# Kernel optimization log

Measured on AMD Instinct MI355X. Metric: run time of the kernel, lower is better.

## Reference

```python
import jax, jax.numpy as jnp
import numpy as np

N_ROWS = 524288   # total ragged rows (sum of lengths)
N_SEG = 128       # number of segments (batch of ragged sequences)
N_FEAT = 256      # num_features
EPS = 1e-05


def setup_inputs() -> dict:
    key = jax.random.key(0)
    k_x = jax.random.fold_in(key, 1)
    x = jax.random.normal(k_x, (N_ROWS, N_FEAT), dtype=jnp.float32)
    # ragged lengths: strictly positive, sum exactly N_ROWS
    rng = np.random.default_rng(0)
    boundaries = np.sort(rng.choice(np.arange(1, N_ROWS), size=N_SEG - 1, replace=False))
    lengths_np = np.diff(np.concatenate([[0], boundaries, [N_ROWS]])).astype(np.int64)
    lengths = jnp.asarray(lengths_np)
    weight = jnp.ones((N_FEAT,), dtype=jnp.float32)
    bias = jnp.zeros((N_FEAT,), dtype=jnp.float32)
    return {"x": x, "lengths": lengths, "weight": weight, "bias": bias}


def reference(x, lengths, weight, bias):
    # instance norm over ragged segments: per-segment, per-feature mean/var
    B = lengths.shape[0]
    seg_ids = jnp.repeat(jnp.arange(B, dtype=jnp.int32), lengths,
                         total_repeat_length=x.shape[0])      # [N]
    cnt = lengths.astype(x.dtype)[:, None]                    # [B,1]
    mean = jax.ops.segment_sum(x, seg_ids, num_segments=B) / cnt          # [B,F]
    x_centered = x - mean[seg_ids]                                        # [N,F]
    var = jax.ops.segment_sum(x_centered * x_centered, seg_ids,
                              num_segments=B) / cnt                       # [B,F]
    std = jnp.sqrt(var + EPS)                                             # [B,F]
    x_norm = x_centered / std[seg_ids]                                    # [N,F]
    return x_norm * weight + bias
```

## Files before the change

### kernel.cpp

```cpp
#include <hip/hip_runtime.h>

#define NFEAT 256
#define NQ    64
#define CH    256
#define BLK   256

typedef float f32x4_native __attribute__((ext_vector_type(4)));

__device__ __forceinline__ void nt_store4(float4* p, float4 v) {
    f32x4_native n; n.x = v.x; n.y = v.y; n.z = v.z; n.w = v.w;
    __builtin_nontemporal_store(n, reinterpret_cast<f32x4_native*>(p));
}

__device__ __forceinline__ void block_scan(const int* __restrict__ lengths, int B,
                                           int* soff, int* sbs) {
    __shared__ int L[BLK], C[BLK];
    const int t = threadIdx.x;
    int len = (t < B) ? lengths[t] : 0;
    L[t] = len;
    C[t] = (len + CH - 1) / CH;
    __syncthreads();
    #pragma unroll
    for (int d = 1; d < BLK; d <<= 1) {
        int a = L[t], c = C[t], aa = 0, cc = 0;
        if (t >= d) { aa = L[t - d]; cc = C[t - d]; }
        __syncthreads();
        L[t] = a + aa; C[t] = c + cc;
        __syncthreads();
    }
    if (t == 0) { soff[0] = 0; sbs[0] = 0; }
    if (t < B)  { soff[t + 1] = L[t]; sbs[t + 1] = C[t]; }
    __syncthreads();
}

__device__ __forceinline__ int find_seg(const int* __restrict__ sbs, int B, int c) {
    __shared__ int sseg;
    const int t = threadIdx.x;
    if (t < B && sbs[t] <= c && c < sbs[t + 1]) sseg = t;
    __syncthreads();
    return sseg;
}

__global__ __launch_bounds__(BLK) void k_partial(const float* __restrict__ x,
                                                 const int* __restrict__ lengths,
                                                 int B,
                                                 float* __restrict__ psum,
                                                 float* __restrict__ psumsq) {
    __shared__ int soff[132], sbs[132];
    block_scan(lengths, B, soff, sbs);

    const int bid = blockIdx.x;
    if (bid >= sbs[B]) return;

    const int seg = find_seg(sbs, B, bid);
    const int r0 = soff[seg] + (bid - sbs[seg]) * CH;
    const int r1 = min(r0 + CH, soff[seg + 1]);

    const int t  = threadIdx.x;
    const int rl = t >> 6;
    const int q  = t & 63;

    float4 sum = make_float4(0.f, 0.f, 0.f, 0.f);
    float4 sq  = make_float4(0.f, 0.f, 0.f, 0.f);

    const float4* x4 = reinterpret_cast<const float4*>(x);
    #pragma unroll 8
    for (int r = r0 + rl; r < r1; r += 4) {
        float4 v = x4[(size_t)r * NQ + q];
        sum.x += v.x; sum.y += v.y; sum.z += v.z; sum.w += v.w;
        sq.x  += v.x * v.x; sq.y += v.y * v.y; sq.z += v.z * v.z; sq.w += v.w * v.w;
    }

    __shared__ float4 lsum[4][NQ];
    __shared__ float4 lsq[4][NQ];
    lsum[rl][q] = sum;
    lsq[rl][q]  = sq;
    __syncthreads();

    if (rl == 0) {
        float4 a0 = lsum[0][q], a1 = lsum[1][q], a2 = lsum[2][q], a3 = lsum[3][q];
        float4 q0 = lsq[0][q],  q1 = lsq[1][q],  q2 = lsq[2][q],  q3 = lsq[3][q];
        float4 ts, tq;
        ts.x = a0.x + a1.x + a2.x + a3.x;  ts.y = a0.y + a1.y + a2.y + a3.y;
        ts.z = a0.z + a1.z + a2.z + a3.z;  ts.w = a0.w + a1.w + a2.w + a3.w;
        tq.x = q0.x + q1.x + q2.x + q3.x;  tq.y = q0.y + q1.y + q2.y + q3.y;
        tq.z = q0.z + q1.z + q2.z + q3.z;  tq.w = q0.w + q1.w + q2.w + q3.w;
        reinterpret_cast<float4*>(psum)[(size_t)bid * NQ + q]   = ts;
        reinterpret_cast<float4*>(psumsq)[(size_t)bid * NQ + q] = tq;
    }
}

__global__ __launch_bounds__(BLK) void k_finalize(const float* __restrict__ psum,
                                                  const float* __restrict__ psumsq,
                                                  const int* __restrict__ lengths,
                                                  int B,
                                                  const float* __restrict__ weight,
                                                  const float* __restrict__ bias,
                                                  float* __restrict__ scale,
                                                  float* __restrict__ shift) {
    __shared__ int soff[132], sbs[132];
    block_scan(lengths, B, soff, sbs);

    const int seg = blockIdx.x;
    const int f   = threadIdx.x;
    const int b0 = sbs[seg], b1 = sbs[seg + 1];

    float s0 = 0.f, s1 = 0.f, s2 = 0.f, s3 = 0.f;
    float q0 = 0.f, q1 = 0.f, q2 = 0.f, q3 = 0.f;
    int b = b0;
    for (; b + 3 < b1; b += 4) {
        s0 += psum[(size_t)(b + 0) * NFEAT + f];  q0 += psumsq[(size_t)(b + 0) * NFEAT + f];
        s1 += psum[(size_t)(b + 1) * NFEAT + f];  q1 += psumsq[(size_t)(b + 1) * NFEAT + f];
        s2 += psum[(size_t)(b + 2) * NFEAT + f];  q2 += psumsq[(size_t)(b + 2) * NFEAT + f];
        s3 += psum[(size_t)(b + 3) * NFEAT + f];  q3 += psumsq[(size_t)(b + 3) * NFEAT + f];
    }
    for (; b < b1; ++b) {
        s0 += psum[(size_t)b * NFEAT + f];
        q0 += psumsq[(size_t)b * NFEAT + f];
    }
    const float s  = (s0 + s1) + (s2 + s3);
    const float qq = (q0 + q1) + (q2 + q3);

    const float cnt  = (float)(soff[seg + 1] - soff[seg]);
    const float m    = s / cnt;
    const float var  = fmaxf(qq / cnt - m * m, 0.f);
    const float rstd = rsqrtf(var + 1e-5f);
    const float sc   = rstd * weight[f];
    scale[(size_t)seg * NFEAT + f] = sc;
    shift[(size_t)seg * NFEAT + f] = bias[f] - m * sc;
}

__global__ __launch_bounds__(BLK) void k_norm(const float* __restrict__ x,
                                              const int* __restrict__ lengths,
                                              int B,
                                              const float* __restrict__ scale,
                                              const float* __restrict__ shift,
                                              float* __restrict__ out) {
    __shared__ int soff[132], sbs[132];
    block_scan(lengths, B, soff, sbs);

    const int nch = sbs[B];
    if ((int)blockIdx.x >= nch) return;
    const int c = nch - 1 - blockIdx.x;

    const int seg = find_seg(sbs, B, c);
    const int r0 = soff[seg] + (c - sbs[seg]) * CH;
    const int r1 = min(r0 + CH, soff[seg + 1]);

    const int t  = threadIdx.x;
    const int rl = t >> 6;
    const int q  = t & 63;

    const float4 sc = reinterpret_cast<const float4*>(scale)[(size_t)seg * NQ + q];
    const float4 sh = reinterpret_cast<const float4*>(shift)[(size_t)seg * NQ + q];

    const float4* x4 = reinterpret_cast<const float4*>(x);
    float4* o4 = reinterpret_cast<float4*>(out);
    #pragma unroll 8
    for (int r = r0 + rl; r < r1; r += 4) {
        const size_t idx = (size_t)r * NQ + q;
        float4 v = x4[idx];
        float4 o;
        o.x = v.x * sc.x + sh.x;
        o.y = v.y * sc.y + sh.y;
        o.z = v.z * sc.z + sh.z;
        o.w = v.w * sc.w + sh.w;
        nt_store4(&o4[idx], o);
    }
}

extern "C" void kernel_launch(void* const* d_in, const int* in_sizes, int n_in,
                              void* d_out, int out_size, void* d_ws, size_t ws_size,
                              hipStream_t stream) {
    const float* x       = (const float*)d_in[0];
    const int*   lengths = (const int*)d_in[1];
    const float* weight  = (const float*)d_in[2];
    const float* bias    = (const float*)d_in[3];
    float*       out     = (float*)d_out;

    const int B = in_sizes[1];
    const int N = in_sizes[0] / NFEAT;
    const int maxCh = N / CH + B;

    char* ws = (char*)d_ws;
    float* scale  = (float*)(ws + 4096);
    float* shift  = scale + (size_t)B * NFEAT;
    float* psum   = shift + (size_t)B * NFEAT;
    float* psumsq = psum + (size_t)maxCh * NFEAT;

    k_partial<<<maxCh, BLK, 0, stream>>>(x, lengths, B, psum, psumsq);
    k_finalize<<<B, BLK, 0, stream>>>(psum, psumsq, lengths, B, weight, bias, scale, shift);
    k_norm<<<maxCh, BLK, 0, stream>>>(x, lengths, B, scale, shift, out);
}
```

Measured before the change: 301.9 us.

## Split stats and normalize passes into three chunk batches for cache reuse

Splits the chunk range into three batches and runs partial-stats, finalize, and normalize per batch. Each normalize launch covers only segments whose statistics completed within the batch, so x read by the stats pass may still be in the last-level cache when it is re-read. This trades one launch per kernel for nine launches, plus extra block scans and idle blocks, in exchange for less DRAM traffic on the second read of x.

```diff
diff --git a/kernel.cpp b/kernel.cpp
--- a/kernel.cpp
+++ b/kernel.cpp
@@ -4,6 +4,7 @@
 #define NQ    64
 #define CH    256
 #define BLK   256
+#define NBATCH 3
 
 typedef float f32x4_native __attribute__((ext_vector_type(4)));
 
@@ -33,27 +34,38 @@
     __syncthreads();
 }
 
-__device__ __forceinline__ int find_seg(const int* __restrict__ sbs, int B, int c) {
-    __shared__ int sseg;
+__device__ __forceinline__ int find_seg(const int* __restrict__ sbs, int B, int c,
+                                        int* slot) {
     const int t = threadIdx.x;
-    if (t < B && sbs[t] <= c && c < sbs[t + 1]) sseg = t;
-    __syncthreads();
-    return sseg;
+    if (t < B && sbs[t] <= c && c < sbs[t + 1]) *slot = t;
+    __syncthreads();
+    return *slot;
+}
+
+__device__ __forceinline__ int cut_chunk(const int* __restrict__ sbs, int B,
+                                         int nch, int phi, int* slot) {
+    if (phi >= nch) return nch;
+    const int t = threadIdx.x;
+    if (t < B && sbs[t] <= phi && phi < sbs[t + 1]) *slot = sbs[t];
+    __syncthreads();
+    return *slot;
 }
 
 __global__ __launch_bounds__(BLK) void k_partial(const float* __restrict__ x,
                                                  const int* __restrict__ lengths,
-                                                 int B,
+                                                 int B, int batch, int cpb,
                                                  float* __restrict__ psum,
                                                  float* __restrict__ psumsq) {
     __shared__ int soff[132], sbs[132];
+    __shared__ int slot0;
     block_scan(lengths, B, soff, sbs);
-
-    const int bid = blockIdx.x;
-    if (bid >= sbs[B]) return;
-
-    const int seg = find_seg(sbs, B, bid);
-    const int r0 = soff[seg] + (bid - sbs[seg]) * CH;
+    const int nch = sbs[B];
+
+    const int c = batch * cpb + blockIdx.x;
+    if (c >= nch) return;
+
+    const int seg = find_seg(sbs, B, c, &slot0);
+    const int r0 = soff[seg] + (c - sbs[seg]) * CH;
     const int r1 = min(r0 + CH, soff[seg + 1]);
 
     const int t  = threadIdx.x;
@@ -85,24 +97,30 @@
         ts.z = a0.z + a1.z + a2.z + a3.z;  ts.w = a0.w + a1.w + a2.w + a3.w;
         tq.x = q0.x + q1.x + q2.x + q3.x;  tq.y = q0.y + q1.y + q2.y + q3.y;
         tq.z = q0.z + q1.z + q2.z + q3.z;  tq.w = q0.w + q1.w + q2.w + q3.w;
-        reinterpret_cast<float4*>(psum)[(size_t)bid * NQ + q]   = ts;
-        reinterpret_cast<float4*>(psumsq)[(size_t)bid * NQ + q] = tq;
+        reinterpret_cast<float4*>(psum)[(size_t)c * NQ + q]   = ts;
+        reinterpret_cast<float4*>(psumsq)[(size_t)c * NQ + q] = tq;
     }
 }
 
 __global__ __launch_bounds__(BLK) void k_finalize(const float* __restrict__ psum,
                                                   const float* __restrict__ psumsq,
                                                   const int* __restrict__ lengths,
-                                                  int B,
+                                                  int B, int batch, int cpb,
                                                   const float* __restrict__ weight,
                                                   const float* __restrict__ bias,
                                                   float* __restrict__ scale,
                                                   float* __restrict__ shift) {
     __shared__ int soff[132], sbs[132];
     block_scan(lengths, B, soff, sbs);
+    const int nch = sbs[B];
 
     const int seg = blockIdx.x;
-    const int f   = threadIdx.x;
+    const int lastc = sbs[seg + 1] - 1;
+    const int plo = batch * cpb;
+    const int phi = min((batch + 1) * cpb, nch);
+    if (lastc < plo || lastc >= phi) return;
+
+    const int f  = threadIdx.x;
     const int b0 = sbs[seg], b1 = sbs[seg + 1];
 
     float s0 = 0.f, s1 = 0.f, s2 = 0.f, s3 = 0.f;
@@ -132,18 +150,24 @@
 
 __global__ __launch_bounds__(BLK) void k_norm(const float* __restrict__ x,
                                               const int* __restrict__ lengths,
-                                              int B,
+                                              int B, int batch, int cpb,
                                               const float* __restrict__ scale,
                                               const float* __restrict__ shift,
                                               float* __restrict__ out) {
     __shared__ int soff[132], sbs[132];
+    __shared__ int slot1, slot2, slot3;
     block_scan(lengths, B, soff, sbs);
-
     const int nch = sbs[B];
-    if ((int)blockIdx.x >= nch) return;
-    const int c = nch - 1 - blockIdx.x;
-
-    const int seg = find_seg(sbs, B, c);
+
+    const int philo = min(batch * cpb, nch);
+    const int phihi = min((batch + 1) * cpb, nch);
+    const int Blo = cut_chunk(sbs, B, nch, philo, &slot1);
+    const int Bhi = cut_chunk(sbs, B, nch, phihi, &slot2);
+
+    const int c = Blo + blockIdx.x;
+    if (c >= Bhi) return;
+
+    const int seg = find_seg(sbs, B, c, &slot3);
     const int r0 = soff[seg] + (c - sbs[seg]) * CH;
     const int r1 = min(r0 + CH, soff[seg + 1]);
 
@@ -181,6 +205,7 @@
     const int B = in_sizes[1];
     const int N = in_sizes[0] / NFEAT;
     const int maxCh = N / CH + B;
+    const int cpb = (maxCh + NBATCH - 1) / NBATCH;
 
     char* ws = (char*)d_ws;
     float* scale  = (float*)(ws + 4096);
@@ -188,7 +213,10 @@
     float* psum   = shift + (size_t)B * NFEAT;
     float* psumsq = psum + (size_t)maxCh * NFEAT;
 
-    k_partial<<<maxCh, BLK, 0, stream>>>(x, lengths, B, psum, psumsq);
-    k_finalize<<<B, BLK, 0, stream>>>(psum, psumsq, lengths, B, weight, bias, scale, shift);
-    k_norm<<<maxCh, BLK, 0, stream>>>(x, lengths, B, scale, shift, out);
-}
+    for (int k = 0; k < NBATCH; ++k) {
+        k_partial<<<cpb, BLK, 0, stream>>>(x, lengths, B, k, cpb, psum, psumsq);
+        k_finalize<<<B, BLK, 0, stream>>>(psum, psumsq, lengths, B, k, cpb,
+                                          weight, bias, scale, shift);
+        k_norm<<<maxCh, BLK, 0, stream>>>(x, lengths, B, k, cpb, scale, shift, out);
+    }
+}
```

After: 325.7 us. +7.9%, slower.
